# Optimization experiments

Measured on AMD Instinct MI355X. Metric: run time of the kernel, lower is better.

## Reference

```python
import jax, jax.numpy as jnp
import numpy as np

N_NODES = 50000
N_EDGES = 800000
HID = 256
MAX_ID = 10000

def _gcn(x, w, b, src, dst, ew, n):
    # PyG GCNConv with self-loops (weight 1.0): out = D^-1/2 (A+I) D^-1/2 (x W) + b
    xw = x @ w                                                   # [N, out]
    deg = jax.ops.segment_sum(ew, dst, num_segments=n) + 1.0     # self-loop adds 1
    dinv = jax.lax.rsqrt(deg)                                    # [N]
    norm = dinv[src] * ew * dinv[dst]                            # [E]
    agg = jax.ops.segment_sum(norm[:, None] * xw[src], dst, num_segments=n)
    agg = agg + (dinv * dinv)[:, None] * xw                      # self-loop term
    return agg + b

def setup_inputs() -> dict:
    key = jax.random.key(0)
    ks = jax.random.split(key, 24)
    s = 0.05
    inp = {
        "node_features": jax.random.normal(ks[0], (N_NODES, 3), jnp.float32),
        "edge_index": jax.random.randint(ks[1], (2, N_EDGES), 0, N_NODES),
        "edge_ids": jax.random.randint(ks[2], (N_EDGES,), 0, MAX_ID + 1),
        "edge_pos": jax.random.randint(ks[3], (N_EDGES,), 0, 3),
        "id_embed": jax.random.normal(ks[4], (MAX_ID + 1, 8), jnp.float32) * s,
        "pos_embed": jax.random.normal(ks[5], (3, 2), jnp.float32) * s,
        "ew_w1": jax.random.normal(ks[6], (10, 10), jnp.float32) * s,
        "ew_b1": jnp.zeros((10,), jnp.float32),
        "ew_w2": jax.random.normal(ks[7], (10, 1), jnp.float32) * s,
        "ew_b2": jnp.zeros((1,), jnp.float32),
        "conv1_w": jax.random.normal(ks[8], (3, HID), jnp.float32) * s,
        "conv1_b": jnp.zeros((HID,), jnp.float32),
        "conv2_w": jax.random.normal(ks[9], (HID, HID), jnp.float32) * s,
        "conv2_b": jnp.zeros((HID,), jnp.float32),
        "actor_w1": jax.random.normal(ks[10], (2 * HID, HID), jnp.float32) * s,
        "actor_b1": jnp.zeros((HID,), jnp.float32),
        "actor_w2": jax.random.normal(ks[11], (HID, 1), jnp.float32) * s,
        "actor_b2": jnp.zeros((1,), jnp.float32),
        "critic_w1": jax.random.normal(ks[12], (2 * HID, 2 * HID), jnp.float32) * s,
        "critic_b1": jnp.zeros((2 * HID,), jnp.float32),
        "critic_w2": jax.random.normal(ks[13], (2 * HID, HID), jnp.float32) * s,
        "critic_b2": jnp.zeros((HID,), jnp.float32),
        "critic_w3": jax.random.normal(ks[14], (HID, 1), jnp.float32) * s,
        "critic_b3": jnp.zeros((1,), jnp.float32),
    }
    return inp

def reference(node_features, edge_index, edge_ids, edge_pos, id_embed, pos_embed,
              ew_w1, ew_b1, ew_w2, ew_b2, conv1_w, conv1_b, conv2_w, conv2_b,
              actor_w1, actor_b1, actor_w2, actor_b2,
              critic_w1, critic_b1, critic_w2, critic_b2, critic_w3, critic_b3):
    n = node_features.shape[0]
    src, dst = edge_index[0], edge_index[1]
    # edge weight MLP: Linear-ReLU-Linear-Sigmoid on [id_embed(8) | pos_embed(2)]
    feat = jnp.concatenate([id_embed[edge_ids], pos_embed[edge_pos]], axis=1)  # [E,10]
    h = jax.nn.relu(feat @ ew_w1 + ew_b1)
    ew = jax.nn.sigmoid(h @ ew_w2 + ew_b2)[:, 0]                               # [E]
    # two GCN layers with ReLU
    x = jax.nn.relu(_gcn(node_features, conv1_w, conv1_b, src, dst, ew, n))
    x = jax.nn.relu(_gcn(x, conv2_w, conv2_b, src, dst, ew, n))
    # global mean pooling + concat
    g = jnp.mean(x, axis=0)                                                    # [H]
    combined = jnp.concatenate([x, jnp.broadcast_to(g, (n, g.shape[0]))], axis=1)
    # actor head
    a = jax.nn.relu(combined @ actor_w1 + actor_b1)
    action_logits = (a @ actor_w2 + actor_b2)[:, 0]                            # [N]
    # critic head on pooled features
    pooled = jnp.mean(combined, axis=0)[None, :]                               # [1,2H]
    c = jax.nn.relu(pooled @ critic_w1 + critic_b1)
    c = jax.nn.relu(c @ critic_w2 + critic_b2)
    state_value = (c @ critic_w3 + critic_b3)[0, 0]                            # scalar
    return action_logits, state_value
```

## Files before the change

kernel.cpp:

```cpp
#include <hip/hip_runtime.h>
#include <math.h>

#define HID 256

typedef __attribute__((ext_vector_type(8))) short short8;
typedef __attribute__((ext_vector_type(4))) float floatx4;

__device__ __forceinline__ ushort bf16_rne(float x) {
    uint u = __float_as_uint(x);
    uint r = (u + 0x7FFFu + ((u >> 16) & 1u)) >> 16;
    return (ushort)r;
}
__device__ __forceinline__ float bf16_to_f(ushort h) {
    return __uint_as_float(((uint)h) << 16);
}

__global__ void k_edge(const int* __restrict__ eid, const int* __restrict__ epos,
                       const float* __restrict__ id_emb, const float* __restrict__ pos_emb,
                       const float* __restrict__ w1, const float* __restrict__ b1,
                       const float* __restrict__ w2, const float* __restrict__ b2,
                       const int* __restrict__ ei, float* __restrict__ ew,
                       float* __restrict__ deg, int* __restrict__ cnt, int E) {
    __shared__ float sW1[100];
    __shared__ float sB1[10];
    __shared__ float sW2[10];
    __shared__ float sB2;
    int t = threadIdx.x;
    if (t < 100) sW1[t] = w1[t];
    if (t < 10) { sB1[t] = b1[t]; sW2[t] = w2[t]; }
    if (t == 0) sB2 = b2[0];
    __syncthreads();
    int e = blockIdx.x * blockDim.x + t;
    if (e >= E) return;
    int id = eid[e];
    int p  = epos[e];
    const float4* ide = (const float4*)(id_emb + (size_t)id * 8);
    float4 fa = ide[0], fb = ide[1];
    float f[10];
    f[0] = fa.x; f[1] = fa.y; f[2] = fa.z; f[3] = fa.w;
    f[4] = fb.x; f[5] = fb.y; f[6] = fb.z; f[7] = fb.w;
    f[8] = pos_emb[p * 2 + 0];
    f[9] = pos_emb[p * 2 + 1];
    float acc = sB2;
#pragma unroll
    for (int j = 0; j < 10; j++) {
        float h = sB1[j];
#pragma unroll
        for (int i = 0; i < 10; i++) h += f[i] * sW1[i * 10 + j];
        h = fmaxf(h, 0.f);
        acc += h * sW2[j];
    }
    float w = 1.f / (1.f + expf(-acc));
    ew[e] = w;
    int dst = ei[E + e];
    atomicAdd(&deg[dst], w);
    atomicAdd(&cnt[dst], 1);
}

__global__ void k_scan_a(const int* __restrict__ cnt, int* __restrict__ row_ptr,
                         int* __restrict__ bsums,
                         float* __restrict__ deg, const float* __restrict__ nf,
                         float4* __restrict__ nf4, float* __restrict__ gsum,
                         const float* __restrict__ w2, const float* __restrict__ aw1,
                         ushort* __restrict__ w2h, ushort* __restrict__ w2l,
                         ushort* __restrict__ a1h, ushort* __restrict__ a1l, int N) {
    __shared__ int s[256];
    int b = blockIdx.x, t = threadIdx.x;
    int i = b * 256 + t;
    if (b == 0) gsum[t] = 0.f;
    if (b < 64) {
        int gid = b * 256 + t;
        int mat = gid >> 13;
        int rem = gid & 8191;
        int c = rem >> 10;
        int tt = (rem >> 6) & 15;
        int L = rem & 63;
        int k0 = 32 * c + (L >> 4) * 8;
        int n  = 16 * tt + (L & 15);
        const float* W = mat ? aw1 : w2;
        ushort* H  = mat ? a1h : w2h;
        ushort* Lo = mat ? a1l : w2l;
        short8 hv, lv;
#pragma unroll
        for (int j = 0; j < 8; j++) {
            float x = W[(size_t)(k0 + j) * HID + n];
            ushort h = bf16_rne(x);
            hv[j] = (short)h;
            lv[j] = (short)bf16_rne(x - bf16_to_f(h));
        }
        size_t off = (size_t)rem * 8;
        *(short8*)(H + off) = hv;
        *(short8*)(Lo + off) = lv;
    }
    if (i < N) {
        deg[i] = 1.f / sqrtf(deg[i] + 1.f);
        nf4[i] = make_float4(nf[i * 3 + 0], nf[i * 3 + 1], nf[i * 3 + 2], 0.f);
    }
    int v = (i < N) ? cnt[i] : 0;
    s[t] = v;
    __syncthreads();
    for (int off = 1; off < 256; off <<= 1) {
        int u = (t >= off) ? s[t - off] : 0;
        __syncthreads();
        s[t] += u;
        __syncthreads();
    }
    int incl = s[t];
    if (i < N) row_ptr[i] = incl - v;
    if (t == 255) bsums[b] = incl;
}

__global__ void k_scan_c(int* __restrict__ row_ptr, int* __restrict__ cursor,
                         const int* __restrict__ bsums, int N, int NB) {
    __shared__ int s[256];
    int b = blockIdx.x, t = threadIdx.x;
    int v = (t < NB) ? bsums[t] : 0;
    s[t] = (t < b) ? v : 0;
    __syncthreads();
    for (int off = 128; off > 0; off >>= 1) {
        if (t < off) s[t] += s[t + off];
        __syncthreads();
    }
    int boff = s[0];
    int i = b * 256 + t;
    if (i < N) {
        int rp = row_ptr[i] + boff;
        row_ptr[i] = rp;
        cursor[i] = rp;
    }
    if (b == NB - 1) {
        __syncthreads();
        s[t] = (t < NB) ? bsums[t] : 0;
        __syncthreads();
        for (int off = 128; off > 0; off >>= 1) {
            if (t < off) s[t] += s[t + off];
            __syncthreads();
        }
        if (t == 0) row_ptr[N] = s[0];
    }
}

__global__ void k_fill(const int* __restrict__ ei, const float* __restrict__ ew,
                       const float* __restrict__ dinv, int* __restrict__ cursor,
                       int2* __restrict__ csr, int E) {
    int e = blockIdx.x * blockDim.x + threadIdx.x;
    if (e >= E) return;
    int src = ei[e];
    int dst = ei[E + e];
    int slot = atomicAdd(&cursor[dst], 1);
    float norm = dinv[src] * ew[e] * dinv[dst];
    csr[slot] = make_int2(src, __float_as_int(norm));
}

__global__ void k_agg3(const int* __restrict__ row_ptr, const int2* __restrict__ csr,
                       const float4* __restrict__ nf4, const float* __restrict__ dinv,
                       float4* __restrict__ T3, int N) {
    int n = blockIdx.x * blockDim.x + threadIdx.x;
    if (n >= N) return;
    int s = row_ptr[n];
    int e = row_ptr[n + 1];
    float ax = 0.f, ay = 0.f, az = 0.f;
    for (int i = s; i < e; i++) {
        int2 sn = csr[i];
        float w = __int_as_float(sn.y);
        float4 v = nf4[sn.x];
        ax = fmaf(w, v.x, ax);
        ay = fmaf(w, v.y, ay);
        az = fmaf(w, v.z, az);
    }
    float d = dinv[n];
    float dd = d * d;
    float4 v = nf4[n];
    ax = fmaf(dd, v.x, ax);
    ay = fmaf(dd, v.y, ay);
    az = fmaf(dd, v.z, az);
    T3[n] = make_float4(ax, ay, az, 0.f);
}

__global__ void k_gatherfused(const int* __restrict__ row_ptr, const int2* __restrict__ csr,
                              const float4* __restrict__ T3, const float* __restrict__ dinv,
                              const float* __restrict__ cw, const float* __restrict__ cb,
                              ushort* __restrict__ Ah, ushort* __restrict__ Al, int N) {
    int lane = threadIdx.x & 63;
    int wv = threadIdx.x >> 6;
    int n = blockIdx.x * 4 + wv;
    if (n >= N) return;
    const float4 w0 = *(const float4*)(cw + 4 * lane);
    const float4 w1 = *(const float4*)(cw + HID + 4 * lane);
    const float4 w2 = *(const float4*)(cw + 2 * HID + 4 * lane);
    const float4 bv = *(const float4*)(cb + 4 * lane);
    int s = row_ptr[n];
    int e = row_ptr[n + 1];
    float4 acc = make_float4(0.f, 0.f, 0.f, 0.f);
    for (int i = s; i < e; i++) {
        int2 sn = csr[i];
        float w = __int_as_float(sn.y);
        float4 t = T3[sn.x];
        float xx = fmaxf(fmaf(t.x, w0.x, fmaf(t.y, w1.x, fmaf(t.z, w2.x, bv.x))), 0.f);
        float xy = fmaxf(fmaf(t.x, w0.y, fmaf(t.y, w1.y, fmaf(t.z, w2.y, bv.y))), 0.f);
        float xz = fmaxf(fmaf(t.x, w0.z, fmaf(t.y, w1.z, fmaf(t.z, w2.z, bv.z))), 0.f);
        float xw = fmaxf(fmaf(t.x, w0.w, fmaf(t.y, w1.w, fmaf(t.z, w2.w, bv.w))), 0.f);
        acc.x = fmaf(w, xx, acc.x);
        acc.y = fmaf(w, xy, acc.y);
        acc.z = fmaf(w, xz, acc.z);
        acc.w = fmaf(w, xw, acc.w);
    }
    float d = dinv[n];
    float dd = d * d;
    float4 t = T3[n];
    float xx = fmaxf(fmaf(t.x, w0.x, fmaf(t.y, w1.x, fmaf(t.z, w2.x, bv.x))), 0.f);
    float xy = fmaxf(fmaf(t.x, w0.y, fmaf(t.y, w1.y, fmaf(t.z, w2.y, bv.y))), 0.f);
    float xz = fmaxf(fmaf(t.x, w0.z, fmaf(t.y, w1.z, fmaf(t.z, w2.z, bv.z))), 0.f);
    float xw = fmaxf(fmaf(t.x, w0.w, fmaf(t.y, w1.w, fmaf(t.z, w2.w, bv.w))), 0.f);
    acc.x = fmaf(dd, xx, acc.x);
    acc.y = fmaf(dd, xy, acc.y);
    acc.z = fmaf(dd, xz, acc.z);
    acc.w = fmaf(dd, xw, acc.w);
    ushort4 hv, lv;
    ushort h;
    h = bf16_rne(acc.x); hv.x = h; lv.x = bf16_rne(acc.x - bf16_to_f(h));
    h = bf16_rne(acc.y); hv.y = h; lv.y = bf16_rne(acc.y - bf16_to_f(h));
    h = bf16_rne(acc.z); hv.z = h; lv.z = bf16_rne(acc.z - bf16_to_f(h));
    h = bf16_rne(acc.w); hv.w = h; lv.w = bf16_rne(acc.w - bf16_to_f(h));
    size_t base = (size_t)n * HID + lane * 4;
    *(ushort4*)(Ah + base) = hv;
    *(ushort4*)(Al + base) = lv;
}

#define ASTRIDE 264

__global__ __launch_bounds__(256, 2) void k_gemm_mfma(
        const ushort* __restrict__ Ah, const ushort* __restrict__ Al,
        const float* __restrict__ b2,
        const ushort* __restrict__ w2h, const ushort* __restrict__ w2l,
        const ushort* __restrict__ a1h, const ushort* __restrict__ a1l,
        float* __restrict__ P, float* __restrict__ gsum, int N) {
    __shared__ ushort Hs[64 * ASTRIDE];
    __shared__ ushort Ls[64 * ASTRIDE];
    int tid = threadIdx.x;
    int n0 = blockIdx.x * 64;
    int w = tid >> 6;
    int L = tid & 63;
    int quad = L >> 4, ln = L & 15;

    int arow[4];
#pragma unroll
    for (int mt = 0; mt < 4; mt++) {
        int r = n0 + mt * 16 + ln;
        arow[mt] = (r < N) ? r : (N - 1);
    }

    floatx4 acc[4][4];
#pragma unroll
    for (int i = 0; i < 4; i++)
#pragma unroll
        for (int j = 0; j < 4; j++) acc[i][j] = 0.f;
    {
        short8 pah[2][4], pal[2][4], pbh[2][4], pbl[2][4];
#pragma unroll
        for (int mt = 0; mt < 4; mt++) {
            size_t ab = (size_t)arow[mt] * HID + quad * 8;
            pah[0][mt] = *(const short8*)(Ah + ab);
            pal[0][mt] = *(const short8*)(Al + ab);
        }
#pragma unroll
        for (int nt = 0; nt < 4; nt++) {
            size_t off = ((size_t)(4 * w + nt) * 64 + L) * 8;
            pbh[0][nt] = *(const short8*)(w2h + off);
            pbl[0][nt] = *(const short8*)(w2l + off);
        }
#pragma unroll
        for (int c = 0; c < 8; c++) {
            int cur = c & 1, nxt = cur ^ 1;
            if (c < 7) {
#pragma unroll
                for (int mt = 0; mt < 4; mt++) {
                    size_t ab = (size_t)arow[mt] * HID + 32 * (c + 1) + quad * 8;
                    pah[nxt][mt] = *(const short8*)(Ah + ab);
                    pal[nxt][mt] = *(const short8*)(Al + ab);
                }
#pragma unroll
                for (int nt = 0; nt < 4; nt++) {
                    size_t off = ((size_t)((c + 1) * 16 + 4 * w + nt) * 64 + L) * 8;
                    pbh[nxt][nt] = *(const short8*)(w2h + off);
                    pbl[nxt][nt] = *(const short8*)(w2l + off);
                }
            }
#pragma unroll
            for (int nt = 0; nt < 4; nt++) {
#pragma unroll
                for (int mt = 0; mt < 4; mt++) {
                    acc[nt][mt] = __builtin_amdgcn_mfma_f32_16x16x32_bf16(pah[cur][mt], pbh[cur][nt], acc[nt][mt], 0, 0, 0);
                    acc[nt][mt] = __builtin_amdgcn_mfma_f32_16x16x32_bf16(pah[cur][mt], pbl[cur][nt], acc[nt][mt], 0, 0, 0);
                    acc[nt][mt] = __builtin_amdgcn_mfma_f32_16x16x32_bf16(pal[cur][mt], pbh[cur][nt], acc[nt][mt], 0, 0, 0);
                }
            }
        }
    }

#pragma unroll
    for (int nt = 0; nt < 4; nt++) {
        int col = (4 * w + nt) * 16 + ln;
        float bb = b2[col];
        float s = 0.f;
#pragma unroll
        for (int mt = 0; mt < 4; mt++) {
#pragma unroll
            for (int r = 0; r < 4; r++) {
                int row = n0 + mt * 16 + quad * 4 + r;
                float v = fmaxf(acc[nt][mt][r] + bb, 0.f);
                acc[nt][mt][r] = v;
                if (row < N) s += v;
            }
        }
        s += __shfl_down(s, 32, 64);
        s += __shfl_down(s, 16, 64);
        if (L < 16) atomicAdd(&gsum[col], s);
    }

#pragma unroll
    for (int nt = 0; nt < 4; nt++) {
        int col = (4 * w + nt) * 16 + ln;
#pragma unroll
        for (int mt = 0; mt < 4; mt++) {
#pragma unroll
            for (int r = 0; r < 4; r++) {
                int row = mt * 16 + quad * 4 + r;
                float v = acc[nt][mt][r];
                ushort h = bf16_rne(v);
                Hs[row * ASTRIDE + col] = h;
                Ls[row * ASTRIDE + col] = bf16_rne(v - bf16_to_f(h));
            }
        }
    }
    __syncthreads();

    floatx4 acc2[4][4];
#pragma unroll
    for (int i = 0; i < 4; i++)
#pragma unroll
        for (int j = 0; j < 4; j++) acc2[i][j] = 0.f;
    {
        short8 pbh[2][4], pbl[2][4];
#pragma unroll
        for (int nt = 0; nt < 4; nt++) {
            size_t off = ((size_t)(4 * w + nt) * 64 + L) * 8;
            pbh[0][nt] = *(const short8*)(a1h + off);
            pbl[0][nt] = *(const short8*)(a1l + off);
        }
#pragma unroll
        for (int c = 0; c < 8; c++) {
            int cur = c & 1, nxt = cur ^ 1;
            if (c < 7) {
#pragma unroll
                for (int nt = 0; nt < 4; nt++) {
                    size_t off = ((size_t)((c + 1) * 16 + 4 * w + nt) * 64 + L) * 8;
                    pbh[nxt][nt] = *(const short8*)(a1h + off);
                    pbl[nxt][nt] = *(const short8*)(a1l + off);
                }
            }
            short8 ahf[4], alf[4];
#pragma unroll
            for (int mt = 0; mt < 4; mt++) {
                int base = (mt * 16 + ln) * ASTRIDE + 32 * c + quad * 8;
                ahf[mt] = *(const short8*)&Hs[base];
                alf[mt] = *(const short8*)&Ls[base];
            }
#pragma unroll
            for (int nt = 0; nt < 4; nt++) {
#pragma unroll
                for (int mt = 0; mt < 4; mt++) {
                    acc2[nt][mt] = __builtin_amdgcn_mfma_f32_16x16x32_bf16(ahf[mt], pbh[cur][nt], acc2[nt][mt], 0, 0, 0);
                    acc2[nt][mt] = __builtin_amdgcn_mfma_f32_16x16x32_bf16(ahf[mt], pbl[cur][nt], acc2[nt][mt], 0, 0, 0);
                    acc2[nt][mt] = __builtin_amdgcn_mfma_f32_16x16x32_bf16(alf[mt], pbh[cur][nt], acc2[nt][mt], 0, 0, 0);
                }
            }
        }
    }

#pragma unroll
    for (int nt = 0; nt < 4; nt++) {
        int col = (4 * w + nt) * 16 + ln;
#pragma unroll
        for (int mt = 0; mt < 4; mt++) {
#pragma unroll
            for (int r = 0; r < 4; r++) {
                int row = n0 + mt * 16 + quad * 4 + r;
                if (row < N) P[(size_t)row * HID + col] = acc2[nt][mt][r];
            }
        }
    }
}

__global__ void k_logits(const float* __restrict__ P, const float* __restrict__ gbias,
                         const float* __restrict__ aw2, const float* __restrict__ ab2,
                         float* __restrict__ out, int N) {
    int lane = threadIdx.x & 63;
    int wv = threadIdx.x >> 6;
    int n = blockIdx.x * 4 + wv;
    if (n >= N) return;
    float4 p = *(const float4*)(P + (size_t)n * HID + 4 * lane);
    float4 gb = *(const float4*)(gbias + 4 * lane);
    float4 w2 = *(const float4*)(aw2 + 4 * lane);
    float v = fmaxf(p.x + gb.x, 0.f) * w2.x
            + fmaxf(p.y + gb.y, 0.f) * w2.y
            + fmaxf(p.z + gb.z, 0.f) * w2.z
            + fmaxf(p.w + gb.w, 0.f) * w2.w;
#pragma unroll
    for (int off = 32; off > 0; off >>= 1) v += __shfl_down(v, off, 64);
    if (lane == 0) out[n] = v + ab2[0];
}

__global__ void k_heads(const float* __restrict__ gsum,
                        const float* __restrict__ aw1, const float* __restrict__ ab1,
                        float* __restrict__ gbias,
                        const float* __restrict__ cw1, const float* __restrict__ cb1,
                        const float* __restrict__ cw2, const float* __restrict__ cb2,
                        const float* __restrict__ cw3, const float* __restrict__ cb3,
                        float* __restrict__ sv_out, float invN) {
    int t = threadIdx.x;
    if (blockIdx.x == 0) {
        if (t < HID) {
            float s = ab1[t];
            for (int j = 0; j < HID; j++) s += gsum[j] * invN * aw1[(HID + j) * HID + t];
            gbias[t] = s;
        }
        return;
    }
    __shared__ float p[2 * HID];
    __shared__ float c1[2 * HID];
    __shared__ float c2[HID];
    p[t] = gsum[t & (HID - 1)] * invN;
    __syncthreads();
    float s = cb1[t];
    for (int i = 0; i < 2 * HID; i++) s += p[i] * cw1[i * 2 * HID + t];
    c1[t] = fmaxf(s, 0.f);
    __syncthreads();
    if (t < HID) {
        float s2 = cb2[t];
        for (int i = 0; i < 2 * HID; i++) s2 += c1[i] * cw2[i * HID + t];
        c2[t] = fmaxf(s2, 0.f) * cw3[t];
    }
    __syncthreads();
    for (int st = HID / 2; st > 0; st >>= 1) {
        if (t < st) c2[t] += c2[t + st];
        __syncthreads();
    }
    if (t == 0) sv_out[0] = c2[0] + cb3[0];
}

extern "C" void kernel_launch(void* const* d_in, const int* in_sizes, int n_in,
                              void* d_out, int out_size, void* d_ws, size_t ws_size,
                              hipStream_t stream) {
    const float* nf      = (const float*)d_in[0];
    const int*   ei      = (const int*)d_in[1];
    const int*   eid     = (const int*)d_in[2];
    const int*   epos    = (const int*)d_in[3];
    const float* id_emb  = (const float*)d_in[4];
    const float* pos_emb = (const float*)d_in[5];
    const float* ew_w1   = (const float*)d_in[6];
    const float* ew_b1   = (const float*)d_in[7];
    const float* ew_w2   = (const float*)d_in[8];
    const float* ew_b2   = (const float*)d_in[9];
    const float* c1w     = (const float*)d_in[10];
    const float* c1b     = (const float*)d_in[11];
    const float* c2w     = (const float*)d_in[12];
    const float* c2b     = (const float*)d_in[13];
    const float* aw1     = (const float*)d_in[14];
    const float* ab1     = (const float*)d_in[15];
    const float* aw2     = (const float*)d_in[16];
    const float* ab2     = (const float*)d_in[17];
    const float* cw1     = (const float*)d_in[18];
    const float* cb1     = (const float*)d_in[19];
    const float* cw2     = (const float*)d_in[20];
    const float* cb2     = (const float*)d_in[21];
    const float* cw3     = (const float*)d_in[22];
    const float* cb3     = (const float*)d_in[23];

    int N = in_sizes[0] / 3;
    int E = in_sizes[2];
    int NB = (N + 255) / 256;
    float invN = 1.f / (float)N;

    char* ws = (char*)d_ws;
    float* deg      = (float*)ws;                         ws += (size_t)N * 4;
    int*   cnt      = (int*)ws;                           ws += (size_t)N * 4;
    float* gsum     = (float*)ws;                         ws += HID * 4;
    ushort* Ah      = (ushort*)ws;                        ws += (size_t)N * HID * 2;
    ushort* Al      = (ushort*)ws;                        ws += (size_t)N * HID * 2;
    float* P        = (float*)ws;                         ws += (size_t)N * HID * 4;
    float* ew       = (float*)ws;                         ws += (size_t)E * 4;
    int2*  csr      = (int2*)ws;                          ws += (size_t)E * 8;
    int*   row_ptr  = (int*)ws;                           ws += (size_t)(N + 1) * 4;
    int*   cursor   = (int*)ws;                           ws += (size_t)N * 4;
    int*   bsums    = (int*)ws;                           ws += 256 * 4;
    float4* T3      = (float4*)ws;                        ws += (size_t)N * 16;
    float4* nf4     = (float4*)ws;                        ws += (size_t)N * 16;
    float* gbias    = (float*)ws;                         ws += HID * 4;
    ushort* w2h     = (ushort*)ws;                        ws += 65536 * 2;
    ushort* w2l     = (ushort*)ws;                        ws += 65536 * 2;
    ushort* a1h     = (ushort*)ws;                        ws += 65536 * 2;
    ushort* a1l     = (ushort*)ws;                        ws += 65536 * 2;

    float* out = (float*)d_out;

    hipMemsetAsync(deg, 0, (size_t)(2 * N) * sizeof(float), stream);

    k_edge<<<(E + 255) / 256, 256, 0, stream>>>(eid, epos, id_emb, pos_emb,
                                                ew_w1, ew_b1, ew_w2, ew_b2, ei, ew, deg, cnt, E);

    k_scan_a<<<NB, 256, 0, stream>>>(cnt, row_ptr, bsums, deg, nf, nf4, gsum,
                                     c2w, aw1, w2h, w2l, a1h, a1l, N);
    k_scan_c<<<NB, 256, 0, stream>>>(row_ptr, cursor, bsums, N, NB);

    k_fill<<<(E + 255) / 256, 256, 0, stream>>>(ei, ew, deg, cursor, csr, E);

    k_agg3<<<(N + 255) / 256, 256, 0, stream>>>(row_ptr, csr, nf4, deg, T3, N);

    k_gatherfused<<<(N + 3) / 4, 256, 0, stream>>>(row_ptr, csr, T3, deg, c1w, c1b, Ah, Al, N);

    k_gemm_mfma<<<(N + 63) / 64, 256, 0, stream>>>(Ah, Al, c2b, w2h, w2l, a1h, a1l, P, gsum, N);

    k_heads<<<2, 2 * HID, 0, stream>>>(gsum, aw1, ab1, gbias,
                                       cw1, cb1, cw2, cb2, cw3, cb3, out + N, invN);

    k_logits<<<(N + 3) / 4, 256, 0, stream>>>(P, gbias, aw2, ab2, out, N);
}
```

Before: 441.6 us.

## Split head MLPs across more blocks and software-prefetch CSR gathers

Replaces the two-block heads kernel with two kernels. The first spreads the critic first layer and the actor global-bias GEMV over 12 blocks with split-K partial sums in shared memory. The second spreads the critic second layer over 4 blocks and reduces the state value with a wave shuffle plus an atomic. The aggregation loops in k_agg3 and k_gatherfused now prefetch the next CSR entry (and its T3 row) one iteration ahead to hide gather latency. The cost is an extra launch and an atomic float add, which makes the state-value summation order nondeterministic.

```diff
diff --git a/kernel.cpp b/kernel.cpp
--- a/kernel.cpp
+++ b/kernel.cpp
@@ -160,13 +160,17 @@
     int s = row_ptr[n];
     int e = row_ptr[n + 1];
     float ax = 0.f, ay = 0.f, az = 0.f;
-    for (int i = s; i < e; i++) {
-        int2 sn = csr[i];
-        float w = __int_as_float(sn.y);
-        float4 v = nf4[sn.x];
-        ax = fmaf(w, v.x, ax);
-        ay = fmaf(w, v.y, ay);
-        az = fmaf(w, v.z, az);
+    if (s < e) {
+        int2 sn = csr[s];
+        for (int i = s; i < e; i++) {
+            int2 snn = (i + 1 < e) ? csr[i + 1] : sn;
+            float w = __int_as_float(sn.y);
+            float4 v = nf4[sn.x];
+            ax = fmaf(w, v.x, ax);
+            ay = fmaf(w, v.y, ay);
+            az = fmaf(w, v.z, az);
+            sn = snn;
+        }
     }
     float d = dinv[n];
     float dd = d * d;
@@ -192,18 +196,31 @@
     int s = row_ptr[n];
     int e = row_ptr[n + 1];
     float4 acc = make_float4(0.f, 0.f, 0.f, 0.f);
-    for (int i = s; i < e; i++) {
-        int2 sn = csr[i];
-        float w = __int_as_float(sn.y);
+    if (s < e) {
+        int2 sn = csr[s];
         float4 t = T3[sn.x];
-        float xx = fmaxf(fmaf(t.x, w0.x, fmaf(t.y, w1.x, fmaf(t.z, w2.x, bv.x))), 0.f);
-        float xy = fmaxf(fmaf(t.x, w0.y, fmaf(t.y, w1.y, fmaf(t.z, w2.y, bv.y))), 0.f);
-        float xz = fmaxf(fmaf(t.x, w0.z, fmaf(t.y, w1.z, fmaf(t.z, w2.z, bv.z))), 0.f);
-        float xw = fmaxf(fmaf(t.x, w0.w, fmaf(t.y, w1.w, fmaf(t.z, w2.w, bv.w))), 0.f);
-        acc.x = fmaf(w, xx, acc.x);
-        acc.y = fmaf(w, xy, acc.y);
-        acc.z = fmaf(w, xz, acc.z);
-        acc.w = fmaf(w, xw, acc.w);
+        for (int i = s; i < e; i++) {
+            int2 snn;
+            float4 tn;
+            if (i + 1 < e) {
+                snn = csr[i + 1];
+                tn = T3[snn.x];
+            } else {
+                snn = sn;
+                tn = t;
+            }
+            float w = __int_as_float(sn.y);
+            float xx = fmaxf(fmaf(t.x, w0.x, fmaf(t.y, w1.x, fmaf(t.z, w2.x, bv.x))), 0.f);
+            float xy = fmaxf(fmaf(t.x, w0.y, fmaf(t.y, w1.y, fmaf(t.z, w2.y, bv.y))), 0.f);
+            float xz = fmaxf(fmaf(t.x, w0.z, fmaf(t.y, w1.z, fmaf(t.z, w2.z, bv.z))), 0.f);
+            float xw = fmaxf(fmaf(t.x, w0.w, fmaf(t.y, w1.w, fmaf(t.z, w2.w, bv.w))), 0.f);
+            acc.x = fmaf(w, xx, acc.x);
+            acc.y = fmaf(w, xy, acc.y);
+            acc.z = fmaf(w, xz, acc.z);
+            acc.w = fmaf(w, xw, acc.w);
+            sn = snn;
+            t = tn;
+        }
     }
     float d = dinv[n];
     float dd = d * d;
@@ -392,6 +409,63 @@
     }
 }
 
+__global__ void k_headsA(const float* __restrict__ gsum,
+                         const float* __restrict__ cw1, const float* __restrict__ cb1,
+                         float* __restrict__ c1g,
+                         const float* __restrict__ aw1, const float* __restrict__ ab1,
+                         float* __restrict__ gbias,
+                         const float* __restrict__ cb3, float* __restrict__ sv_out,
+                         float invN) {
+    __shared__ float part[4][64];
+    int b = blockIdx.x, t = threadIdx.x;
+    int c = t & 63;
+    int kr = t >> 6;
+    if (b == 0 && t == 0) sv_out[0] = cb3[0];
+    if (b < 8) {
+        int col = b * 64 + c;
+        float s = 0.f;
+        for (int k = kr * 128; k < kr * 128 + 128; k++)
+            s += gsum[k & (HID - 1)] * invN * cw1[(size_t)k * 512 + col];
+        part[kr][c] = s;
+        __syncthreads();
+        if (kr == 0) {
+            float v = cb1[col] + part[0][c] + part[1][c] + part[2][c] + part[3][c];
+            c1g[col] = fmaxf(v, 0.f);
+        }
+    } else {
+        int col = (b - 8) * 64 + c;
+        float s = 0.f;
+        for (int k = kr * 64; k < kr * 64 + 64; k++)
+            s += gsum[k] * invN * aw1[(size_t)(HID + k) * HID + col];
+        part[kr][c] = s;
+        __syncthreads();
+        if (kr == 0)
+            gbias[col] = ab1[col] + part[0][c] + part[1][c] + part[2][c] + part[3][c];
+    }
+}
+
+__global__ void k_headsB(const float* __restrict__ c1g,
+                         const float* __restrict__ cw2, const float* __restrict__ cb2,
+                         const float* __restrict__ cw3, float* __restrict__ sv_out) {
+    __shared__ float part[4][64];
+    int b = blockIdx.x, t = threadIdx.x;
+    int c = t & 63;
+    int kr = t >> 6;
+    int col = b * 64 + c;
+    float s = 0.f;
+    for (int k = kr * 128; k < kr * 128 + 128; k++)
+        s += c1g[k] * cw2[(size_t)k * HID + col];
+    part[kr][c] = s;
+    __syncthreads();
+    if (kr == 0) {
+        float v = fmaxf(cb2[col] + part[0][c] + part[1][c] + part[2][c] + part[3][c], 0.f)
+                * cw3[col];
+#pragma unroll
+        for (int off = 32; off > 0; off >>= 1) v += __shfl_down(v, off, 64);
+        if (c == 0) atomicAdd(sv_out, v);
+    }
+}
+
 __global__ void k_logits(const float* __restrict__ P, const float* __restrict__ gbias,
                          const float* __restrict__ aw2, const float* __restrict__ ab2,
                          float* __restrict__ out, int N) {
@@ -409,44 +483,6 @@
 #pragma unroll
     for (int off = 32; off > 0; off >>= 1) v += __shfl_down(v, off, 64);
     if (lane == 0) out[n] = v + ab2[0];
-}
-
-__global__ void k_heads(const float* __restrict__ gsum,
-                        const float* __restrict__ aw1, const float* __restrict__ ab1,
-                        float* __restrict__ gbias,
-                        const float* __restrict__ cw1, const float* __restrict__ cb1,
-                        const float* __restrict__ cw2, const float* __restrict__ cb2,
-                        const float* __restrict__ cw3, const float* __restrict__ cb3,
-                        float* __restrict__ sv_out, float invN) {
-    int t = threadIdx.x;
-    if (blockIdx.x == 0) {
-        if (t < HID) {
-            float s = ab1[t];
-            for (int j = 0; j < HID; j++) s += gsum[j] * invN * aw1[(HID + j) * HID + t];
-            gbias[t] = s;
-        }
-        return;
-    }
-    __shared__ float p[2 * HID];
-    __shared__ float c1[2 * HID];
-    __shared__ float c2[HID];
-    p[t] = gsum[t & (HID - 1)] * invN;
-    __syncthreads();
-    float s = cb1[t];
-    for (int i = 0; i < 2 * HID; i++) s += p[i] * cw1[i * 2 * HID + t];
-    c1[t] = fmaxf(s, 0.f);
-    __syncthreads();
-    if (t < HID) {
-        float s2 = cb2[t];
-        for (int i = 0; i < 2 * HID; i++) s2 += c1[i] * cw2[i * HID + t];
-        c2[t] = fmaxf(s2, 0.f) * cw3[t];
-    }
-    __syncthreads();
-    for (int st = HID / 2; st > 0; st >>= 1) {
-        if (t < st) c2[t] += c2[t + st];
-        __syncthreads();
-    }
-    if (t == 0) sv_out[0] = c2[0] + cb3[0];
 }
 
 extern "C" void kernel_launch(void* const* d_in, const int* in_sizes, int n_in,
@@ -497,6 +533,7 @@
     float4* T3      = (float4*)ws;                        ws += (size_t)N * 16;
     float4* nf4     = (float4*)ws;                        ws += (size_t)N * 16;
     float* gbias    = (float*)ws;                         ws += HID * 4;
+    float* c1g      = (float*)ws;                         ws += 512 * 4;
     ushort* w2h     = (ushort*)ws;                        ws += 65536 * 2;
     ushort* w2l     = (ushort*)ws;                        ws += 65536 * 2;
     ushort* a1h     = (ushort*)ws;                        ws += 65536 * 2;
@@ -521,8 +558,9 @@
 
     k_gemm_mfma<<<(N + 63) / 64, 256, 0, stream>>>(Ah, Al, c2b, w2h, w2l, a1h, a1l, P, gsum, N);
 
-    k_heads<<<2, 2 * HID, 0, stream>>>(gsum, aw1, ab1, gbias,
-                                       cw1, cb1, cw2, cb2, cw3, cb3, out + N, invN);
+    k_headsA<<<12, 256, 0, stream>>>(gsum, cw1, cb1, c1g, aw1, ab1, gbias,
+                                     cb3, out + N, invN);
+    k_headsB<<<4, 256, 0, stream>>>(c1g, cw2, cb2, cw3, out + N);
 
     k_logits<<<(N + 3) / 4, 256, 0, stream>>>(P, gbias, aw2, ab2, out, N);
 }
```

Measured after the change: 435.1 us. Within noise of the previous version (-1.5%).
